# Kernel optimization log

Hardware: AMD Instinct MI355X
Metric: run time of the kernel (lower is better)

## Reference

```python
import jax, jax.numpy as jnp
import numpy as np

N_MELS = 20
NUM_FRAMES = 32
FRAME_LEN = 512
SR = NUM_FRAMES * FRAME_LEN  # 16384
EPS = np.finfo(np.float64).eps  # matches np.finfo(float).eps in original


def _mel_filters(n_fft, sr, n_mels, fmin, fmax):
    """Replicates librosa.filters.mel(..., htk=False, norm=None) in pure numpy."""
    f_sp = 200.0 / 3.0
    min_log_hz = 1000.0
    min_log_mel = min_log_hz / f_sp
    logstep = np.log(6.4) / 27.0

    def hz_to_mel(f):
        f = np.asarray(f, dtype=np.float64)
        return np.where(f >= min_log_hz,
                        min_log_mel + np.log(np.maximum(f, 1e-10) / min_log_hz) / logstep,
                        f / f_sp)

    def mel_to_hz(m):
        m = np.asarray(m, dtype=np.float64)
        return np.where(m >= min_log_mel,
                        min_log_hz * np.exp(logstep * (m - min_log_mel)),
                        f_sp * m)

    fftfreqs = np.linspace(0.0, sr / 2.0, 1 + n_fft // 2)
    mels = np.linspace(hz_to_mel(fmin), hz_to_mel(fmax), n_mels + 2)
    mel_f = mel_to_hz(mels)
    fdiff = np.diff(mel_f)
    ramps = mel_f[:, None] - fftfreqs[None, :]
    lower = -ramps[:-2] / fdiff[:-1, None]
    upper = ramps[2:] / fdiff[1:, None]
    weights = np.maximum(0.0, np.minimum(lower, upper))  # norm=None -> no scaling
    return weights.astype(np.float32)  # (n_mels, 1+n_fft//2)


def setup_inputs() -> dict:
    key = jax.random.key(0)
    inputs = jax.random.normal(key, (4096, NUM_FRAMES, FRAME_LEN), dtype=jnp.float32)
    filter_banks = jnp.asarray(_mel_filters(FRAME_LEN, SR, N_MELS, 0.0, SR / 2.0 + 1.0))
    hw = jnp.asarray(np.hamming(FRAME_LEN).astype(np.float32))
    return {"inputs": inputs, "filter_banks": filter_banks, "hw": hw}


def reference(inputs, filter_banks, hw):
    # Hamming window + forward-normalized rFFT; original squares only the REAL part.
    fft_real = jnp.fft.rfft(inputs * hw, norm="forward").real  # (B, 32, 257)
    mag = fft_real * fft_real
    mels = jnp.einsum("mf,btf->btm", filter_banks, mag)  # (B, 32, 20)
    mels = jnp.where(mels == 0, jnp.float32(EPS), mels)
    log_mels = jnp.log2(mels)
    return jnp.floor(log_mels)[..., None]  # (B, 32, 20, 1)
```

## Files before the change

### kernel.cpp

```cpp
#include <hip/hip_runtime.h>
#include <math.h>


#define MARGIN_L2 1.0e-3f
#define IDX(e) ((e) + ((e) >> 3))

__device__ __forceinline__ float4 f4add(float4 a, float4 b) {
    return make_float4(a.x + b.x, a.y + b.y, a.z + b.z, a.w + b.w);
}
__device__ __forceinline__ float4 f4sub(float4 a, float4 b) {
    return make_float4(a.x - b.x, a.y - b.y, a.z - b.z, a.w - b.w);
}
__device__ __forceinline__ float4 cmulc4(float2 w, float4 z) {
    return make_float4(w.x * z.x + w.y * z.y, w.x * z.y - w.y * z.x,
                       w.x * z.z + w.y * z.w, w.x * z.w - w.y * z.z);
}

__device__ __forceinline__ void bfly4(int s, int l, const float2* tw,
                                      float4 x1, float4 y1, float4 x2, float4 y2,
                                      float4* dst) {
    const int j = l >> s;
    const int r = l & ((1 << s) - 1);
    const float2 w1 = tw[j << (s + 1)];
    const float2 w2 = tw[j << (s + 2)];
    const float4 u1 = f4add(x1, y1);
    const float4 v1 = cmulc4(w1, f4sub(x1, y1));
    const float4 u2 = f4add(x2, y2);
    const float4 m  = cmulc4(w1, f4sub(x2, y2));
    const float4 v2 = make_float4(m.y, -m.x, m.w, -m.z);
    const float4 o0 = f4add(u1, u2);
    const float4 o1 = cmulc4(w2, f4sub(u1, u2));
    const float4 o2 = f4add(v1, v2);
    const float4 o3 = cmulc4(w2, f4sub(v1, v2));
    const int eb = (j << (s + 2)) + r;
    dst[IDX(eb)]            = o0;
    dst[IDX(eb + (1 << s))] = o2;
    dst[IDX(eb + (2 << s))] = o1;
    dst[IDX(eb + (3 << s))] = o3;
}

__global__ void prep_full(const float* __restrict__ fb,
                          double* __restrict__ tw64,
                          float2* __restrict__ tw32,
                          float* __restrict__ fbP,
                          unsigned* count) {
    const int t = threadIdx.x;
    double s, c;
    sincospi((double)t * (1.0 / 256.0), &s, &c);
    tw64[t]       = c;
    tw64[256 + t] = s;
    tw32[t] = make_float2((float)c, (float)s);
    for (int i = t; i < 20 * 264; i += 256) {
        const int m = i / 264, k = i % 264;
        fbP[i] = (k < 257) ? fb[m * 257 + k] : 0.0f;
    }
    if (count && t == 0) *count = 0;
}

__global__ void prep_tw64(double* __restrict__ tw64) {
    const int t = threadIdx.x;
    double s, c;
    sincospi((double)t * (1.0 / 256.0), &s, &c);
    tw64[t]       = c;
    tw64[256 + t] = s;
}

__global__ __launch_bounds__(256, 4) void phase1(
    const float* __restrict__ x,
    const float* __restrict__ hw,
    const float2* __restrict__ tw32,
    const float* __restrict__ fbP,
    float* __restrict__ out,
    unsigned* __restrict__ count,
    unsigned* __restrict__ worklist)
{
    __shared__ __align__(16) float4 Abuf[4][288];
    __shared__ __align__(16) float4 Bbuf[4][288];
    __shared__ __align__(16) float2 tw[256];

    const int t = threadIdx.x;
    const int w = t >> 6;
    const int l = t & 63;
    const int fg0 = (blockIdx.x * 4 + w) * 2;
    const int fg1 = fg0 + 1;

    tw[t] = tw32[t];
    __syncthreads();

    float4* A = &Abuf[w][0];
    float4* B = &Bbuf[w][0];

    {
        const float2* xa = (const float2*)(x + (size_t)fg0 * 512);
        const float2* xb = (const float2*)(x + (size_t)fg1 * 512);
        const float2* hp = (const float2*)hw;
        const float2 h0 = hp[l],       h1 = hp[l + 64];
        const float2 h2 = hp[l + 128], h3 = hp[l + 192];
        const float2 a0 = xa[l],       a1 = xa[l + 64];
        const float2 a2 = xa[l + 128], a3 = xa[l + 192];
        const float2 b0 = xb[l],       b1 = xb[l + 64];
        const float2 b2 = xb[l + 128], b3 = xb[l + 192];
        const float4 x1 = make_float4(a0.x * h0.x, a0.y * h0.y,
                                      b0.x * h0.x, b0.y * h0.y);
        const float4 x2 = make_float4(a1.x * h1.x, a1.y * h1.y,
                                      b1.x * h1.x, b1.y * h1.y);
        const float4 y1 = make_float4(a2.x * h2.x, a2.y * h2.y,
                                      b2.x * h2.x, b2.y * h2.y);
        const float4 y2 = make_float4(a3.x * h3.x, a3.y * h3.y,
                                      b3.x * h3.x, b3.y * h3.y);
        bfly4(0, l, tw, x1, y1, x2, y2, B);
    }
    __builtin_amdgcn_wave_barrier();

    float4* src = B;
    float4* dst = A;
#pragma unroll
    for (int s = 2; s <= 6; s += 2) {
        const float4 x1 = src[IDX(l)];
        const float4 y1 = src[IDX(l + 128)];
        const float4 x2 = src[IDX(l + 64)];
        const float4 y2 = src[IDX(l + 192)];
        bfly4(s, l, tw, x1, y1, x2, y2, dst);
        __builtin_amdgcn_wave_barrier();
        float4* tmp = src; src = dst; dst = tmp;
    }

    float2* pwr2 = (float2*)B;
    {
        const float4* Z = A;
#pragma unroll
        for (int i = 0; i < 4; i++) {
            const int k = l + 64 * i;
            const float4 zk = Z[IDX(k)];
            const float4 zc = Z[IDX((256 - k) & 255)];
            const float2 wk = tw[k];
            const float rexA = 0.5f * (zk.x + zc.x)
                             + 0.5f * (wk.x * (zk.y + zc.y) - wk.y * (zk.x - zc.x));
            const float rexB = 0.5f * (zk.z + zc.z)
                             + 0.5f * (wk.x * (zk.w + zc.w) - wk.y * (zk.z - zc.z));
            const float vA = rexA * (1.0f / 512.0f);
            const float vB = rexB * (1.0f / 512.0f);
            pwr2[k] = make_float2(vA * vA, vB * vB);
        }
        if (l == 0) {
            const float4 z0 = Z[IDX(0)];
            const float vA = (z0.x - z0.y) * (1.0f / 512.0f);
            const float vB = (z0.z - z0.w) * (1.0f / 512.0f);
            pwr2[256] = make_float2(vA * vA, vB * vB);
        }
        if (l >= 57) pwr2[257 + (l - 57)] = make_float2(0.0f, 0.0f);
    }
    __builtin_amdgcn_wave_barrier();

    float accA = 0.0f, accB = 0.0f;
    if (l < 60) {
        const int mel = l % 20;
        const int sub = l / 20;
        const float4* fb4 = (const float4*)(fbP + mel * 264) + sub * 22;
        const float4* pw4 = (const float4*)pwr2 + sub * 44;
#pragma unroll
        for (int it = 0; it < 22; it++) {
            const float4 w4 = fb4[it];
            const float4 q0 = pw4[2 * it];
            const float4 q1 = pw4[2 * it + 1];
            accA = fmaf(w4.w, q1.z, fmaf(w4.z, q1.x,
                   fmaf(w4.y, q0.z, fmaf(w4.x, q0.x, accA))));
            accB = fmaf(w4.w, q1.w, fmaf(w4.z, q1.y,
                   fmaf(w4.y, q0.w, fmaf(w4.x, q0.y, accB))));
        }
    }
    const float pA1 = __shfl(accA, l + 20);
    const float pA2 = __shfl(accA, l + 40);
    const float pB1 = __shfl(accB, l + 20);
    const float pB2 = __shfl(accB, l + 40);

    int flagA = 0, flagB = 0;
    if (l < 20) {
        const float vA = accA + pA1 + pA2;
        float flA;
        if (vA < 1e-30f) { flA = -52.0f; flagA = 1; }
        else {
            const float l2 = log2f(vA);
            flA = floorf(l2);
            flagA = (l2 - flA < MARGIN_L2) | ((flA + 1.0f - l2) < MARGIN_L2);
        }
        out[(size_t)fg0 * 20 + l] = flA;

        const float vB = accB + pB1 + pB2;
        float flB;
        if (vB < 1e-30f) { flB = -52.0f; flagB = 1; }
        else {
            const float l2 = log2f(vB);
            flB = floorf(l2);
            flagB = (l2 - flB < MARGIN_L2) | ((flB + 1.0f - l2) < MARGIN_L2);
        }
        out[(size_t)fg1 * 20 + l] = flB;
    }
    const unsigned long long bA = __ballot(flagA);
    const unsigned long long bB = __ballot(flagB);
    if (l == 0) {
        const unsigned nf = (bA != 0ULL) + (bB != 0ULL);
        if (nf) {
            unsigned idx = atomicAdd(count, nf);
            if (bA != 0ULL) worklist[idx++] = (unsigned)fg0;
            if (bB != 0ULL) worklist[idx]   = (unsigned)fg1;
        }
    }
}

__global__ __launch_bounds__(256) void phase2_wl(
    const float* __restrict__ x,
    const float* __restrict__ fb,
    const float* __restrict__ hw,
    const double* __restrict__ tw64,
    const unsigned* __restrict__ count,
    const unsigned* __restrict__ worklist,
    float* __restrict__ out)
{
    __shared__ double Are[256], Aim[256], Bre[256], Bim[256];
    __shared__ double ltc[256], lts[256];
    __shared__ double pwr[257];

    const int t = threadIdx.x;
    ltc[t] = tw64[t];
    lts[t] = tw64[256 + t];
    __syncthreads();

    const unsigned n = *count;
    for (unsigned i = blockIdx.x; i < n; i += gridDim.x) {
        const int f = (int)worklist[i];

        {
            const float2 xv = ((const float2*)x)[(size_t)f * 256 + t];
            const float2 hv = ((const float2*)hw)[t];
            Are[t] = (double)xv.x * (double)hv.x;
            Aim[t] = (double)xv.y * (double)hv.y;
        }
        __syncthreads();

        double* sre = Are; double* sim = Aim;
        double* dre = Bre; double* dim = Bim;
        const int p = t & 127;
        const int which = t >> 7;
#pragma unroll
        for (int s = 0; s < 8; s++) {
            const int j = p >> s;
            const double ar = sre[p],       ai = sim[p];
            const double br = sre[p + 128], bi = sim[p + 128];
            double orr, oi;
            int dpos;
            if (which) {
                const int idx = j << (s + 1);
                const double wr = ltc[idx];
                const double wi = -lts[idx];
                const double ur = ar - br, ui = ai - bi;
                orr = wr * ur - wi * ui;
                oi  = wr * ui + wi * ur;
                dpos = p + ((j + 1) << s);
            } else {
                orr = ar + br;
                oi  = ai + bi;
                dpos = p + (j << s);
            }
            dre[dpos] = orr;
            dim[dpos] = oi;
            __syncthreads();
            double* tmp;
            tmp = sre; sre = dre; dre = tmp;
            tmp = sim; sim = dim; dim = tmp;
        }

        {
            const double a = sre[t], b = sim[t];
            const int t2 = (256 - t) & 255;
            const double c = sre[t2], d = sim[t2];
            const double rex = 0.5 * (a + c)
                             + 0.5 * (ltc[t] * (b + d) - lts[t] * (a - c));
            const double v = rex * (1.0 / 512.0);
            pwr[t] = v * v;
            if (t == 0) {
                const double vn = (a - b) * (1.0 / 512.0);
                pwr[256] = vn * vn;
            }
        }
        __syncthreads();

        if (t < 160) {
            const int mel = t >> 3;
            const int sub = t & 7;
            const float* wrow = fb + mel * 257;
            double acc = 0.0;
            for (int k = sub; k < 257; k += 8)
                acc = fma((double)wrow[k], pwr[k], acc);
            acc += __shfl_down(acc, 4, 8);
            acc += __shfl_down(acc, 2, 8);
            acc += __shfl_down(acc, 1, 8);
            if (sub == 0) {
                double v = acc;
                if (v == 0.0) v = 2.220446049250313e-16;
                out[(size_t)f * 20 + mel] = (float)floor(log2(v));
            }
        }
        __syncthreads();
    }
}

__global__ __launch_bounds__(256) void f64_all(
    const float*  __restrict__ x,
    const float*  __restrict__ fb,
    const float*  __restrict__ hw,
    const double* __restrict__ tw,
    float* __restrict__ out)
{
    __shared__ double Are[256], Aim[256], Bre[256], Bim[256];
    __shared__ double ltc[256], lts[256];
    __shared__ double pwr[257];

    const int t = threadIdx.x;
    const int f = blockIdx.x;

    ltc[t] = tw[t];
    lts[t] = tw[256 + t];
    {
        const float2 xv = ((const float2*)x)[(size_t)f * 256 + t];
        const float2 hv = ((const float2*)hw)[t];
        Are[t] = (double)xv.x * (double)hv.x;
        Aim[t] = (double)xv.y * (double)hv.y;
    }
    __syncthreads();

    double* sre = Are; double* sim = Aim;
    double* dre = Bre; double* dim = Bim;
    const int p = t & 127;
    const int which = t >> 7;
#pragma unroll
    for (int s = 0; s < 8; s++) {
        const int j = p >> s;
        const double ar = sre[p],       ai = sim[p];
        const double br = sre[p + 128], bi = sim[p + 128];
        double orr, oi;
        int dpos;
        if (which) {
            const int idx = j << (s + 1);
            const double wr = ltc[idx];
            const double wi = -lts[idx];
            const double ur = ar - br, ui = ai - bi;
            orr = wr * ur - wi * ui;
            oi  = wr * ui + wi * ur;
            dpos = p + ((j + 1) << s);
        } else {
            orr = ar + br;
            oi  = ai + bi;
            dpos = p + (j << s);
        }
        dre[dpos] = orr;
        dim[dpos] = oi;
        __syncthreads();
        double* tmp;
        tmp = sre; sre = dre; dre = tmp;
        tmp = sim; sim = dim; dim = tmp;
    }

    {
        const double a = sre[t], b = sim[t];
        const int t2 = (256 - t) & 255;
        const double c = sre[t2], d = sim[t2];
        const double rex = 0.5 * (a + c)
                         + 0.5 * (ltc[t] * (b + d) - lts[t] * (a - c));
        const double v = rex * (1.0 / 512.0);
        pwr[t] = v * v;
        if (t == 0) {
            const double vn = (a - b) * (1.0 / 512.0);
            pwr[256] = vn * vn;
        }
    }
    __syncthreads();

    if (t < 160) {
        const int mel = t >> 3;
        const int sub = t & 7;
        const float* wrow = fb + mel * 257;
        double acc = 0.0;
        for (int k = sub; k < 257; k += 8)
            acc = fma((double)wrow[k], pwr[k], acc);
        acc += __shfl_down(acc, 4, 8);
        acc += __shfl_down(acc, 2, 8);
        acc += __shfl_down(acc, 1, 8);
        if (sub == 0) {
            double v = acc;
            if (v == 0.0) v = 2.220446049250313e-16;
            out[(size_t)f * 20 + mel] = (float)floor(log2(v));
        }
    }
}

extern "C" void kernel_launch(void* const* d_in, const int* in_sizes, int n_in,
                              void* d_out, int out_size, void* d_ws, size_t ws_size,
                              hipStream_t stream) {
    const float* x  = (const float*)d_in[0];
    const float* fb = (const float*)d_in[1];
    const float* hw = (const float*)d_in[2];
    float* out = (float*)d_out;

    const int frames = in_sizes[0] / 512;

    char* ws = (char*)d_ws;
    double* tw64 = (double*)ws;
    float2* tw32 = (float2*)(ws + 4096);
    float*  fbP  = (float*)(ws + 6144);

    const size_t T1 = 32832 + 4 * (size_t)frames;

    if (ws_size >= T1 && (frames % 8) == 0) {
        unsigned* count    = (unsigned*)(ws + 32768);
        unsigned* worklist = (unsigned*)(ws + 32832);
        prep_full<<<1, 256, 0, stream>>>(fb, tw64, tw32, fbP, count);
        phase1<<<frames / 8, 256, 0, stream>>>(x, hw, tw32, fbP, out,
                                               count, worklist);
        phase2_wl<<<4096, 256, 0, stream>>>(x, fb, hw, tw64, count, worklist, out);
    } else {
        prep_tw64<<<1, 256, 0, stream>>>(tw64);
        f64_all<<<frames, 256, 0, stream>>>(x, fb, hw, tw64, out);
    }
}
```

Baseline: 458.9 us.

## Use single in-place LDS buffer, specialize last FFT stage, exploit conjugate symmetry

Replaces the ping-pong A/B shared buffers with one in-place buffer per wave, halving LDS usage so more blocks can reside per CU, and raises the launch-bounds occupancy hint from 4 to 7. The final radix-4 stage is special-cased with trivial twiddles. The real-FFT post-processing now computes bins k and 256-k together from one pair of loads, halving LDS reads in that step. The in-place scheme relies on wave barriers and correct read-before-write ordering within each wave, and the higher occupancy hint may constrain registers.

```diff
diff --git a/kernel.cpp b/kernel.cpp
--- a/kernel.cpp
+++ b/kernel.cpp
@@ -65,7 +65,7 @@
     tw64[256 + t] = s;
 }
 
-__global__ __launch_bounds__(256, 4) void phase1(
+__global__ __launch_bounds__(256, 7) void phase1(
     const float* __restrict__ x,
     const float* __restrict__ hw,
     const float2* __restrict__ tw32,
@@ -74,8 +74,7 @@
     unsigned* __restrict__ count,
     unsigned* __restrict__ worklist)
 {
-    __shared__ __align__(16) float4 Abuf[4][288];
-    __shared__ __align__(16) float4 Bbuf[4][288];
+    __shared__ __align__(16) float4 buf[4][288];
     __shared__ __align__(16) float2 tw[256];
 
     const int t = threadIdx.x;
@@ -87,8 +86,7 @@
     tw[t] = tw32[t];
     __syncthreads();
 
-    float4* A = &Abuf[w][0];
-    float4* B = &Bbuf[w][0];
+    float4* const W = &buf[w][0];
 
     {
         const float2* xa = (const float2*)(x + (size_t)fg0 * 512);
@@ -108,45 +106,79 @@
                                       b2.x * h2.x, b2.y * h2.y);
         const float4 y2 = make_float4(a3.x * h3.x, a3.y * h3.y,
                                       b3.x * h3.x, b3.y * h3.y);
-        bfly4(0, l, tw, x1, y1, x2, y2, B);
+        bfly4(0, l, tw, x1, y1, x2, y2, W);
     }
     __builtin_amdgcn_wave_barrier();
 
-    float4* src = B;
-    float4* dst = A;
 #pragma unroll
-    for (int s = 2; s <= 6; s += 2) {
-        const float4 x1 = src[IDX(l)];
-        const float4 y1 = src[IDX(l + 128)];
-        const float4 x2 = src[IDX(l + 64)];
-        const float4 y2 = src[IDX(l + 192)];
-        bfly4(s, l, tw, x1, y1, x2, y2, dst);
+    for (int s = 2; s <= 4; s += 2) {
+        const float4 x1 = W[IDX(l)];
+        const float4 y1 = W[IDX(l + 128)];
+        const float4 x2 = W[IDX(l + 64)];
+        const float4 y2 = W[IDX(l + 192)];
+        bfly4(s, l, tw, x1, y1, x2, y2, W);
         __builtin_amdgcn_wave_barrier();
-        float4* tmp = src; src = dst; dst = tmp;
-    }
-
-    float2* pwr2 = (float2*)B;
+    }
     {
-        const float4* Z = A;
-#pragma unroll
-        for (int i = 0; i < 4; i++) {
-            const int k = l + 64 * i;
-            const float4 zk = Z[IDX(k)];
-            const float4 zc = Z[IDX((256 - k) & 255)];
-            const float2 wk = tw[k];
-            const float rexA = 0.5f * (zk.x + zc.x)
-                             + 0.5f * (wk.x * (zk.y + zc.y) - wk.y * (zk.x - zc.x));
-            const float rexB = 0.5f * (zk.z + zc.z)
-                             + 0.5f * (wk.x * (zk.w + zc.w) - wk.y * (zk.z - zc.z));
-            const float vA = rexA * (1.0f / 512.0f);
-            const float vB = rexB * (1.0f / 512.0f);
-            pwr2[k] = make_float2(vA * vA, vB * vB);
+        const float4 x1 = W[IDX(l)];
+        const float4 y1 = W[IDX(l + 128)];
+        const float4 x2 = W[IDX(l + 64)];
+        const float4 y2 = W[IDX(l + 192)];
+        const float4 u1 = f4add(x1, y1);
+        const float4 v1 = f4sub(x1, y1);
+        const float4 u2 = f4add(x2, y2);
+        const float4 m  = f4sub(x2, y2);
+        const float4 v2 = make_float4(m.y, -m.x, m.w, -m.z);
+        W[IDX(l)]       = f4add(u1, u2);
+        W[IDX(l + 64)]  = f4add(v1, v2);
+        W[IDX(l + 128)] = f4sub(u1, u2);
+        W[IDX(l + 192)] = f4sub(v1, v2);
+    }
+    __builtin_amdgcn_wave_barrier();
+
+    float2* const pwr2 = (float2*)W;
+    {
+        const float4 zk0 = W[IDX(l)];
+        const float4 zc0 = W[IDX((256 - l) & 255)];
+        const float4 zk1 = W[IDX(l + 64)];
+        const float4 zc1 = W[IDX(192 - l)];
+        const float4 zm  = W[IDX(128)];
+        const float2 w0 = tw[l];
+        const float2 w1 = tw[l + 64];
+        __builtin_amdgcn_wave_barrier();
+
+        {
+            const float SrA = zk0.x + zc0.x, SiA = zk0.y + zc0.y;
+            const float DrA = zk0.x - zc0.x;
+            const float SrB = zk0.z + zc0.z, SiB = zk0.w + zc0.w;
+            const float DrB = zk0.z - zc0.z;
+            const float EA = 0.5f * SrA, TA = 0.5f * (w0.x * SiA - w0.y * DrA);
+            const float EB = 0.5f * SrB, TB = 0.5f * (w0.x * SiB - w0.y * DrB);
+            const float aA = (EA + TA) * (1.0f / 512.0f);
+            const float aB = (EB + TB) * (1.0f / 512.0f);
+            const float bA = (EA - TA) * (1.0f / 512.0f);
+            const float bB = (EB - TB) * (1.0f / 512.0f);
+            pwr2[l]       = make_float2(aA * aA, aB * aB);
+            pwr2[256 - l] = make_float2(bA * bA, bB * bB);
+        }
+        {
+            const float SrA = zk1.x + zc1.x, SiA = zk1.y + zc1.y;
+            const float DrA = zk1.x - zc1.x;
+            const float SrB = zk1.z + zc1.z, SiB = zk1.w + zc1.w;
+            const float DrB = zk1.z - zc1.z;
+            const float EA = 0.5f * SrA, TA = 0.5f * (w1.x * SiA - w1.y * DrA);
+            const float EB = 0.5f * SrB, TB = 0.5f * (w1.x * SiB - w1.y * DrB);
+            const float aA = (EA + TA) * (1.0f / 512.0f);
+            const float aB = (EB + TB) * (1.0f / 512.0f);
+            const float bA = (EA - TA) * (1.0f / 512.0f);
+            const float bB = (EB - TB) * (1.0f / 512.0f);
+            pwr2[l + 64]  = make_float2(aA * aA, aB * aB);
+            pwr2[192 - l] = make_float2(bA * bA, bB * bB);
         }
         if (l == 0) {
-            const float4 z0 = Z[IDX(0)];
-            const float vA = (z0.x - z0.y) * (1.0f / 512.0f);
-            const float vB = (z0.z - z0.w) * (1.0f / 512.0f);
-            pwr2[256] = make_float2(vA * vA, vB * vB);
+            const float vA = zm.x * (1.0f / 512.0f);
+            const float vB = zm.z * (1.0f / 512.0f);
+            pwr2[128] = make_float2(vA * vA, vB * vB);
         }
         if (l >= 57) pwr2[257 + (l - 57)] = make_float2(0.0f, 0.0f);
     }
```

Result: no change. 455.5 us (-0.7%).
